# Optimization experiments

Hardware: AMD Instinct MI355X
Metric: run time of the kernel (lower is better)

## Reference

```python
import jax, jax.numpy as jnp
import numpy as np

N_USER = 20000
N_ITEM = 20000
N = N_USER + N_ITEM          # total nodes
D = 128                      # n_hid (= in_feats = out_feats)
H = 4                        # GAT heads
L = 2                        # n_layers
M = 8                        # mem_size (hypernet bottleneck)
T = 5                        # num_rels in MemoryLayer
E_UI = 40000                 # user->item bipartite edges
E_T = 16000                  # homogeneous edges per relation type (grouped)
EPS = 1e-5


def _layer_norm(x, w, b):
    mu = x.mean(-1, keepdims=True)
    var = ((x - mu) ** 2).mean(-1, keepdims=True)
    return (x - mu) * jax.lax.rsqrt(var + EPS) * w + b


def _gat(h_src, h_dst, src_idx, dst_idx, n_dst, W, al, ar, bias):
    """DGL GATConv (shared fc, eval-mode dropout=identity, elu activation)."""
    fs = (h_src @ W.T).reshape(-1, H, D)          # [Ns, H, D]
    fd = (h_dst @ W.T).reshape(-1, H, D)          # [Nd, H, D]
    el = (fs * al).sum(-1)                        # [Ns, H]
    er = (fd * ar).sum(-1)                        # [Nd, H]
    e = jax.nn.leaky_relu(el[src_idx] + er[dst_idx], 0.2)   # [E, H]
    emax = jax.ops.segment_max(e, dst_idx, num_segments=n_dst)
    ex = jnp.exp(e - emax[dst_idx])
    denom = jax.ops.segment_sum(ex, dst_idx, num_segments=n_dst)
    a = ex / denom[dst_idx]                       # edge softmax per dst
    rst = jax.ops.segment_sum(a[:, :, None] * fs[src_idx], dst_idx, num_segments=n_dst)
    return jax.nn.elu(rst + bias.reshape(1, H, D))           # [Nd, H, D]


def _memory_layer(feat, edge_src, edge_dst, Wc, bc, Ww, nWc, nbc, nWw, h_bias, ln_w, ln_b):
    # edges grouped by relation type: edge_src/edge_dst are [T, E_T]
    hs = feat[edge_src]                           # [T, Et, D]
    hd = feat[edge_dst]                           # [T, Et, D]
    # per-edge hypernetwork: coef = LeakyReLU(Linear(dst)); w = Ww(coef); msg = w @ src
    coef = jax.nn.leaky_relu(jnp.einsum('ted,tmd->tem', hd, Wc) + bc[:, None, :], 0.2)
    tmp = jnp.einsum('tei,tmoi->temo', hs, Ww)    # [T, Et, M, D] -- M-bottleneck path
    msg = jnp.einsum('tem,temo->teo', coef, tmp)  # [T, Et, D]
    flat_dst = edge_dst.reshape(-1)
    s = jax.ops.segment_sum(msg.reshape(-1, D), flat_dst, num_segments=N)
    cnt = jax.ops.segment_sum(jnp.ones((flat_dst.shape[0],), feat.dtype), flat_dst, num_segments=N)
    agg = s / jnp.maximum(cnt, 1.0)[:, None]      # fn.mean (0 for isolated nodes)
    rep = _layer_norm(agg, ln_w, ln_b) + h_bias
    # self-loop node_ME(feat, feat)
    ncoef = jax.nn.leaky_relu(feat @ nWc.T + nbc, 0.2)       # [N, M]
    ntmp = jnp.einsum('ni,moi->nmo', feat, nWw)              # [N, M, D]
    rep = rep + jnp.einsum('nm,nmo->no', ncoef, ntmp)
    return jax.nn.leaky_relu(rep, 0.2)            # dropout = identity (eval)


def setup_inputs() -> dict:
    key = jax.random.key(0)
    ks = jax.random.split(key, 16)
    s = 0.05
    return {
        "embedding": jax.random.normal(ks[0], (N, D), jnp.float32),
        "gat_fc_W": jax.random.normal(ks[1], (L, 2, H * D, D), jnp.float32) * s,
        "gat_attn_l": jax.random.normal(ks[2], (L, 2, H, D), jnp.float32) * s,
        "gat_attn_r": jax.random.normal(ks[3], (L, 2, H, D), jnp.float32) * s,
        "gat_bias": jnp.zeros((L, 2, H * D), jnp.float32),
        "proj_W": jax.random.normal(ks[4], (L, 2, D, H * D), jnp.float32) * s,
        "proj_b": jnp.zeros((L, 2, D), jnp.float32),
        "mem_rel_Wc": jax.random.normal(ks[5], (L, T, M, D), jnp.float32) * s,
        "mem_rel_bc": jnp.zeros((L, T, M), jnp.float32),
        "mem_rel_Ww": jax.random.normal(ks[6], (L, T, M, D, D), jnp.float32) * s,
        "mem_node_Wc": jax.random.normal(ks[7], (L, M, D), jnp.float32) * s,
        "mem_node_bc": jnp.zeros((L, M), jnp.float32),
        "mem_node_Ww": jax.random.normal(ks[8], (L, M, D, D), jnp.float32) * s,
        "mem_h_bias": jnp.zeros((L, D), jnp.float32),
        "mem_ln_w": jnp.ones((L, D), jnp.float32),
        "mem_ln_b": jnp.zeros((L, D), jnp.float32),
        "final_ln_w": jnp.ones(((L + 1) * D,), jnp.float32),
        "final_ln_b": jnp.zeros(((L + 1) * D,), jnp.float32),
        "src_u": jax.random.randint(ks[9], (E_UI,), 0, N_USER, jnp.int32),
        "dst_i": jax.random.randint(ks[10], (E_UI,), 0, N_ITEM, jnp.int32),
        "edge_src": jax.random.randint(ks[11], (T, E_T), 0, N, jnp.int32),
        "edge_dst": jax.random.randint(ks[12], (T, E_T), 0, N, jnp.int32),
    }


def reference(embedding, gat_fc_W, gat_attn_l, gat_attn_r, gat_bias, proj_W, proj_b,
              mem_rel_Wc, mem_rel_bc, mem_rel_Ww, mem_node_Wc, mem_node_bc, mem_node_Ww,
              mem_h_bias, mem_ln_w, mem_ln_b, final_ln_w, final_ln_b,
              src_u, dst_i, edge_src, edge_dst):
    features = embedding
    all_emb = [features]
    for l in range(L):
        hu, hi = features[:N_USER], features[N_USER:]
        # relation 0: item -> user (dst = user)
        gu = _gat(hi, hu, dst_i, src_u, N_USER,
                  gat_fc_W[l, 0], gat_attn_l[l, 0], gat_attn_r[l, 0], gat_bias[l, 0])
        ru = jax.nn.elu(gu.reshape(N_USER, H * D) @ proj_W[l, 0].T + proj_b[l, 0])
        # relation 1: user -> item (dst = item)
        gi = _gat(hu, hi, src_u, dst_i, N_ITEM,
                  gat_fc_W[l, 1], gat_attn_l[l, 1], gat_attn_r[l, 1], gat_bias[l, 1])
        ri = jnp.asarray(jax.nn.elu(gi.reshape(N_ITEM, H * D) @ proj_W[l, 1].T + proj_b[l, 1]))
        trans = jnp.concatenate([ru, ri], axis=0)             # [N, D]
        mem = _memory_layer(all_emb[-1], edge_src, edge_dst,
                            mem_rel_Wc[l], mem_rel_bc[l], mem_rel_Ww[l],
                            mem_node_Wc[l], mem_node_bc[l], mem_node_Ww[l],
                            mem_h_bias[l], mem_ln_w[l], mem_ln_b[l])
        features = mem + trans
        all_emb.append(features)
    return _layer_norm(jnp.concatenate(all_emb, axis=1), final_ln_w, final_ln_b)
```

## Files before the change

kernel.cpp:

```cpp
#include <hip/hip_runtime.h>
#include <hip/hip_bf16.h>
#include <math.h>

typedef __hip_bfloat16 bf16;

#define NUSER 20000
#define NITEM 20000
#define NTOT  40000
#define DD    128
#define HH    4
#define TT    5
#define MMEM  8
#define EUI   40000
#define ET    16000

#define MP_N  40064
#define MP_H  20096

typedef __attribute__((ext_vector_type(8))) short short8;
typedef __attribute__((ext_vector_type(4))) float f32x4;

__device__ __forceinline__ void gload16(const bf16* g, bf16* l){
  __builtin_amdgcn_global_load_lds(
      (const __attribute__((address_space(1))) unsigned int*)g,
      (__attribute__((address_space(3))) unsigned int*)l, 16, 0, 0);
}
__device__ __forceinline__ float bu2f_lo(unsigned u){ return __uint_as_float(u << 16); }
__device__ __forceinline__ float bu2f_hi(unsigned u){ return __uint_as_float(u & 0xffff0000u); }

__device__ __forceinline__ int stage_cg(int lane){
  return (((lane&3) ^ ((lane>>2)&3) ^ (lane>>4)) << 3);
}
__device__ __forceinline__ int read_pc8(int lm, int lq){
  return ((lq ^ (lm&3) ^ ((lm>>2)&3)) << 3);
}

__global__ __launch_bounds__(256) void k_mfma_gemm(
    const bf16* __restrict__ A, const bf16* __restrict__ B,
    const float* __restrict__ bias, float* __restrict__ C,
    long Astr, long Bstr, long biasStr, long Cstr,
    int ldc, int M, int K, int act, int accum)
{
  A += (size_t)blockIdx.z*Astr; B += (size_t)blockIdx.z*Bstr;
  if (bias) bias += (size_t)blockIdx.z*biasStr;
  C += (size_t)blockIdx.z*Cstr;
  __shared__ bf16 As[3][4096];
  __shared__ bf16 Bs[3][4096];
  int tid = threadIdx.x;
  int wave = tid >> 6, lane = tid & 63;
  int r0 = blockIdx.x * 128, c0 = blockIdx.y * 128;
  int wm = (wave >> 1) * 64, wn = (wave & 1) * 64;
  f32x4 acc[4][4];
  #pragma unroll
  for (int i=0;i<4;i++)
    #pragma unroll
    for (int j=0;j<4;j++) acc[i][j] = (f32x4){0.f,0.f,0.f,0.f};

  int rq = lane >> 2;
  int cg = stage_cg(lane);
  const bf16* Ag = A + (size_t)(r0 + wave*32 + rq)*K + cg;
  const bf16* Bg = B + (size_t)(c0 + wave*32 + rq)*K + cg;
  int lm = lane & 15, lq = lane >> 4;
  int pc8 = read_pc8(lm, lq);

  int ns = K >> 5;
  {
    bf16* dA = &As[0][wave*1024]; bf16* dB = &Bs[0][wave*1024];
    gload16(Ag,        dA); gload16(Ag + 16*K, dA + 512);
    gload16(Bg,        dB); gload16(Bg + 16*K, dB + 512);
  }
  if (ns > 1){
    bf16* dA = &As[1][wave*1024]; bf16* dB = &Bs[1][wave*1024];
    gload16(Ag + 32,        dA); gload16(Ag + 16*K + 32, dA + 512);
    gload16(Bg + 32,        dB); gload16(Bg + 16*K + 32, dB + 512);
    asm volatile("s_waitcnt vmcnt(4)" ::: "memory");
  } else {
    asm volatile("s_waitcnt vmcnt(0)" ::: "memory");
  }
  __builtin_amdgcn_s_barrier();

  int cur = 0, stg = 2;
  for (int i = 0; i < ns; i++){
    if (i + 2 < ns){
      int k2 = (i + 2) << 5;
      bf16* dA = &As[stg][wave*1024]; bf16* dB = &Bs[stg][wave*1024];
      gload16(Ag + k2,        dA); gload16(Ag + 16*K + k2, dA + 512);
      gload16(Bg + k2,        dB); gload16(Bg + 16*K + k2, dB + 512);
    }
    const bf16* Ard = &As[cur][(wm + lm)*32 + pc8];
    const bf16* Brd = &Bs[cur][(wn + lm)*32 + pc8];
    short8 af[4], bfv[4];
    #pragma unroll
    for (int ii=0;ii<4;ii++) af[ii]  = *(const short8*)(Ard + ii*16*32);
    #pragma unroll
    for (int j=0;j<4;j++)    bfv[j]  = *(const short8*)(Brd + j*16*32);
    #pragma unroll
    for (int ii=0;ii<4;ii++)
      #pragma unroll
      for (int j=0;j<4;j++)
        acc[ii][j] = __builtin_amdgcn_mfma_f32_16x16x32_bf16(af[ii], bfv[j], acc[ii][j], 0, 0, 0);
    if (i < ns - 1){
      if (i + 2 < ns) asm volatile("s_waitcnt vmcnt(4)" ::: "memory");
      else            asm volatile("s_waitcnt vmcnt(0)" ::: "memory");
      __builtin_amdgcn_s_barrier();
    }
    cur = (cur == 2) ? 0 : cur + 1;
    stg = (stg == 2) ? 0 : stg + 1;
  }
  #pragma unroll
  for (int i=0;i<4;i++){
    #pragma unroll
    for (int j=0;j<4;j++){
      int c = c0 + wn + j*16 + lm;
      #pragma unroll
      for (int rg=0; rg<4; rg++){
        int r = r0 + wm + i*16 + lq*4 + rg;
        if (r < M){
          float v = acc[i][j][rg];
          if (bias) v += bias[c];
          if (act==1) v = v>0.f ? v : expm1f(v);
          float* cp = &C[(size_t)r*ldc + c];
          if (accum) *cp += v; else *cp = v;
        }
      }
    }
  }
}

__global__ __launch_bounds__(256) void k_fc_gemm(
    const bf16* __restrict__ A, const bf16* __restrict__ B,
    bf16* __restrict__ Fb, const float* __restrict__ al, const float* __restrict__ ar,
    float* __restrict__ el, float* __restrict__ er, int M)
{
  __shared__ bf16 As[3][4096];
  __shared__ bf16 Bs[3][4096];
  __shared__ float redE[2][2][128];
  int tid = threadIdx.x;
  int wave = tid >> 6, lane = tid & 63;
  int h = blockIdx.y;
  int r0 = blockIdx.x * 128;
  int wm = (wave >> 1) * 64, wn = (wave & 1) * 64;
  f32x4 acc[4][4];
  #pragma unroll
  for (int i=0;i<4;i++)
    #pragma unroll
    for (int j=0;j<4;j++) acc[i][j] = (f32x4){0.f,0.f,0.f,0.f};

  int rq = lane >> 2;
  int cg = stage_cg(lane);
  const bf16* Ag = A + (size_t)(r0 + wave*32 + rq)*128 + cg;
  const bf16* Bg = B + (size_t)(h*128 + wave*32 + rq)*128 + cg;
  int lm = lane & 15, lq = lane >> 4;
  int pc8 = read_pc8(lm, lq);

  {
    bf16* dA = &As[0][wave*1024]; bf16* dB = &Bs[0][wave*1024];
    gload16(Ag,            dA); gload16(Ag + 16*128, dA + 512);
    gload16(Bg,            dB); gload16(Bg + 16*128, dB + 512);
  }
  {
    bf16* dA = &As[1][wave*1024]; bf16* dB = &Bs[1][wave*1024];
    gload16(Ag + 32,       dA); gload16(Ag + 16*128 + 32, dA + 512);
    gload16(Bg + 32,       dB); gload16(Bg + 16*128 + 32, dB + 512);
  }
  asm volatile("s_waitcnt vmcnt(4)" ::: "memory");
  __builtin_amdgcn_s_barrier();

  #pragma unroll
  for (int i = 0; i < 4; i++){
    if (i + 2 < 4){
      const int k2 = (i + 2) << 5;
      bf16* dA = &As[(i+2)%3][wave*1024]; bf16* dB = &Bs[(i+2)%3][wave*1024];
      gload16(Ag + k2,        dA); gload16(Ag + 16*128 + k2, dA + 512);
      gload16(Bg + k2,        dB); gload16(Bg + 16*128 + k2, dB + 512);
    }
    const bf16* Ard = &As[i%3][(wm + lm)*32 + pc8];
    const bf16* Brd = &Bs[i%3][(wn + lm)*32 + pc8];
    short8 af[4], bfv[4];
    #pragma unroll
    for (int ii=0;ii<4;ii++) af[ii]  = *(const short8*)(Ard + ii*16*32);
    #pragma unroll
    for (int j=0;j<4;j++)    bfv[j]  = *(const short8*)(Brd + j*16*32);
    #pragma unroll
    for (int ii=0;ii<4;ii++)
      #pragma unroll
      for (int j=0;j<4;j++)
        acc[ii][j] = __builtin_amdgcn_mfma_f32_16x16x32_bf16(af[ii], bfv[j], acc[ii][j], 0, 0, 0);
    if (i < 3){
      if (i + 2 < 4) asm volatile("s_waitcnt vmcnt(4)" ::: "memory");
      else           asm volatile("s_waitcnt vmcnt(0)" ::: "memory");
      __builtin_amdgcn_s_barrier();
    }
  }
  float alv[4], arv[4];
  #pragma unroll
  for (int j=0;j<4;j++){
    int c = h*128 + wn + j*16 + lm;
    alv[j] = al[c]; arv[j] = ar[c];
  }
  int wnh = wave & 1;
  #pragma unroll
  for (int i=0;i<4;i++){
    #pragma unroll
    for (int rg=0; rg<4; rg++){
      float se = 0.f, sr = 0.f;
      #pragma unroll
      for (int j=0;j<4;j++){
        float v = acc[i][j][rg];
        se = fmaf(v, alv[j], se);
        sr = fmaf(v, arv[j], sr);
      }
      #pragma unroll
      for (int msk=1; msk<16; msk<<=1){
        se += __shfl_xor(se, msk);
        sr += __shfl_xor(sr, msk);
      }
      if (lm == 0){
        int rl = wm + i*16 + lq*4 + rg;
        redE[0][wnh][rl] = se;
        redE[1][wnh][rl] = sr;
      }
    }
  }
  #pragma unroll
  for (int i=0;i<4;i++){
    #pragma unroll
    for (int j=0;j<4;j++){
      int c = h*128 + wn + j*16 + lm;
      #pragma unroll
      for (int rg=0; rg<4; rg++){
        int r = r0 + wm + i*16 + lq*4 + rg;
        if (r < M) Fb[(size_t)r*512 + c] = __float2bfloat16(acc[i][j][rg]);
      }
    }
  }
  __syncthreads();
  if (tid < 128){
    int r = r0 + tid;
    if (r < M) el[(size_t)r*4 + h] = redE[0][0][tid] + redE[0][1][tid];
  } else {
    int t2 = tid - 128;
    int r = r0 + t2;
    if (r < M) er[(size_t)r*4 + h] = redE[1][0][t2] + redE[1][1][t2];
  }
}

__global__ __launch_bounds__(256) void k_memgemm(
    const float* __restrict__ feat, const int* __restrict__ src,
    const float* __restrict__ coef, const bf16* __restrict__ B,
    float* __restrict__ C, bf16* __restrict__ Cb,
    const float* __restrict__ trans, float* __restrict__ fout,
    long srcStr, long coefStr, long Bstr, long CbStr,
    int Mvalid, int mode)
{
  __shared__ bf16 Af[64*136];
  __shared__ float cfS[8*64];
  __shared__ bf16 Bs[3][2][4096];
  int t = blockIdx.y;
  const int*   srcT  = src ? src + (size_t)t*srcStr : nullptr;
  const float* coefT = coef + (size_t)t*coefStr;
  const bf16*  Bt    = B + (size_t)t*Bstr;
  int tid = threadIdx.x, wave = tid >> 6, lane = tid & 63;
  int r0 = blockIdx.x * 64;

  {
    int rL = tid >> 2, seg = tid & 3;
    int r = r0 + rL;
    bool valid = r < Mvalid;
    int s = valid ? (srcT ? srcT[r] : r) : 0;
    const float4* fp = (const float4*)(feat + (size_t)s*128 + seg*32);
    bf16* ap = Af + rL*136 + seg*32;
    #pragma unroll
    for (int q=0;q<8;q+=2){
      float4 v0 = fp[q], v1 = fp[q+1];
      *(__hip_bfloat162*)(ap + q*4)     = __float22bfloat162_rn(make_float2(v0.x, v0.y));
      *(__hip_bfloat162*)(ap + q*4 + 2) = __float22bfloat162_rn(make_float2(v0.z, v0.w));
      *(__hip_bfloat162*)(ap + q*4 + 4) = __float22bfloat162_rn(make_float2(v1.x, v1.y));
      *(__hip_bfloat162*)(ap + q*4 + 6) = __float22bfloat162_rn(make_float2(v1.z, v1.w));
    }
  }
  if (tid < 64){
    int r = r0 + tid;
    bool valid = r < Mvalid;
    #pragma unroll
    for (int m=0;m<8;m++)
      cfS[m*64 + tid] = valid ? coefT[(size_t)r*8 + m] : 0.f;
  }

  int rq = lane >> 2;
  int cg = stage_cg(lane);
  const bf16* Bg0 = Bt + (size_t)(wave*32 + rq)*1024 + cg;
  const bf16* Bg1 = Bt + (size_t)(wave*32 + 16 + rq)*1024 + cg;
  int wm = (wave >> 1) * 32, wn = (wave & 1) * 64;
  int lm = lane & 15, lq = lane >> 4;
  int pc8 = read_pc8(lm, lq);

  #pragma unroll
  for (int p0=0; p0<2; p0++){
    #pragma unroll
    for (int h=0; h<2; h++){
      int kk = p0*2 + h;
      bf16* d = &Bs[p0][h][wave*1024];
      gload16(Bg0 + kk*32, d);
      gload16(Bg1 + kk*32, d + 512);
    }
  }
  asm volatile("s_waitcnt lgkmcnt(0) vmcnt(4)" ::: "memory");
  __builtin_amdgcn_s_barrier();

  short8 afr[4][2];
  #pragma unroll
  for (int ic=0; ic<4; ic++)
    #pragma unroll
    for (int i=0; i<2; i++)
      afr[ic][i] = *(const short8*)(Af + (size_t)(wm + i*16 + lm)*136 + ic*32 + lq*8);

  f32x4 accC[2][4];
  #pragma unroll
  for (int i=0;i<2;i++)
    #pragma unroll
    for (int j=0;j<4;j++) accC[i][j] = (f32x4){0.f,0.f,0.f,0.f};
  f32x4 accM[2][4];

  #pragma unroll
  for (int p = 0; p < 16; p++){
    if (p + 2 < 16){
      #pragma unroll
      for (int h=0; h<2; h++){
        const int kk = (p+2)*2 + h;
        bf16* d = &Bs[(p+2)%3][h][wave*1024];
        gload16(Bg0 + kk*32, d);
        gload16(Bg1 + kk*32, d + 512);
      }
    }
    #pragma unroll
    for (int h=0; h<2; h++){
      const int kk = p*2 + h;
      const int ic = kk & 3;
      const bf16* bb = &Bs[p%3][h][0];
      short8 bfv[4];
      #pragma unroll
      for (int j=0;j<4;j++)
        bfv[j] = *(const short8*)(bb + (wn + lm + j*16)*32 + pc8);
      if (ic == 0){
        #pragma unroll
        for (int i=0;i<2;i++)
          #pragma unroll
          for (int j=0;j<4;j++)
            accM[i][j] = __builtin_amdgcn_mfma_f32_16x16x32_bf16(afr[0][i], bfv[j],
                             (f32x4){0.f,0.f,0.f,0.f}, 0, 0, 0);
      } else {
        #pragma unroll
        for (int i=0;i<2;i++)
          #pragma unroll
          for (int j=0;j<4;j++)
            accM[i][j] = __builtin_amdgcn_mfma_f32_16x16x32_bf16(afr[ic][i], bfv[j], accM[i][j], 0, 0, 0);
      }
    }
    if (p & 1){
      const int m = p >> 1;
      #pragma unroll
      for (int i=0;i<2;i++){
        f32x4 cf4 = *(const f32x4*)(cfS + m*64 + wm + i*16 + lq*4);
        #pragma unroll
        for (int j=0;j<4;j++)
          #pragma unroll
          for (int rg=0; rg<4; rg++)
            accC[i][j][rg] = fmaf(cf4[rg], accM[i][j][rg], accC[i][j][rg]);
      }
    }
    if (p < 15){
      if (p + 2 < 16) asm volatile("s_waitcnt vmcnt(4)" ::: "memory");
      else            asm volatile("s_waitcnt vmcnt(0)" ::: "memory");
      __builtin_amdgcn_s_barrier();
    }
  }

  #pragma unroll
  for (int i=0;i<2;i++){
    #pragma unroll
    for (int j=0;j<4;j++){
      int c = wn + j*16 + lm;
      #pragma unroll
      for (int rg=0; rg<4; rg++){
        int r = r0 + wm + i*16 + lq*4 + rg;
        if (r < Mvalid){
          float v = accC[i][j][rg];
          if (mode == 0){
            Cb[(size_t)t*CbStr + (size_t)r*128 + c] = __float2bfloat16(v);
          } else {
            float x = C[(size_t)r*128 + c] + v;
            x = x>0.f ? x : 0.2f*x;
            fout[(size_t)r*128 + c] = x + trans[(size_t)r*128 + c];
          }
        }
      }
    }
  }
}

__global__ void k_f2b(const float* __restrict__ in, bf16* __restrict__ o, int nv, int nt){
  int i = blockIdx.x*256 + threadIdx.x;
  if (i < nt) o[i] = __float2bfloat16(i < nv ? in[i] : 0.f);
}

__global__ void k_repack(const float* __restrict__ in, bf16* __restrict__ o){
  int s = blockIdx.y;
  int g = blockIdx.x*256 + threadIdx.x;
  int m = g >> 14, od = (g >> 7) & 127, i = g & 127;
  o[(size_t)s*131072 + (size_t)od*1024 + m*128 + i] = __float2bfloat16(in[(size_t)s*131072 + g]);
}

__global__ void k_hist(const int* __restrict__ dIdx, int* __restrict__ cnt, int E){
  int e = blockIdx.x*256+threadIdx.x;
  if (e<E) atomicAdd(&cnt[dIdx[e]], 1);
}

__global__ __launch_bounds__(1024) void k_scan(const int* __restrict__ in,
                                               int* __restrict__ out, int n){
  __shared__ int wsum[16];
  __shared__ int carry;
  int tidx = threadIdx.x, lane = tidx & 63, w = tidx >> 6;
  if (tidx == 0) carry = 0;
  __syncthreads();
  for (int base = 0; base < n; base += 1024){
    int i = base + tidx;
    int v = (i < n) ? in[i] : 0;
    int x = v;
    #pragma unroll
    for (int off = 1; off < 64; off <<= 1){
      int t = __shfl_up(x, off);
      if (lane >= off) x += t;
    }
    if (lane == 63) wsum[w] = x;
    __syncthreads();
    if (w == 0 && lane < 16){
      int t = wsum[lane];
      #pragma unroll
      for (int off=1; off<16; off<<=1){
        int u = __shfl_up(t, off, 16);
        if (lane >= off) t += u;
      }
      wsum[lane] = t;
    }
    __syncthreads();
    int woff = (w == 0) ? 0 : wsum[w-1];
    int excl = carry + woff + x - v;
    if (i < n) out[i] = excl;
    __syncthreads();
    if (tidx == 1023) carry = carry + wsum[15];
    __syncthreads();
  }
  if (tidx == 0) out[n] = carry;
}

__global__ void k_csr_scatter(const int* __restrict__ sIdx, const int* __restrict__ dIdx,
                              int sOff, const int* __restrict__ rowptr,
                              int* __restrict__ cursor, int* __restrict__ col, int E){
  int e = blockIdx.x*256+threadIdx.x; if (e>=E) return;
  int d = dIdx[e];
  int pos = rowptr[d] + atomicAdd(&cursor[d], 1);
  col[pos] = sIdx[e] + sOff;
}

__global__ void k_csr_scatter_eid(const int* __restrict__ dIdx, const int* __restrict__ rowptr,
                                  int* __restrict__ cursor, int* __restrict__ col, int E){
  int e = blockIdx.x*256+threadIdx.x; if (e>=E) return;
  int d = dIdx[e];
  int pos = rowptr[d] + atomicAdd(&cursor[d], 1);
  col[pos] = e;
}

__global__ __launch_bounds__(64) void k_gat_gather(
    const int* __restrict__ rowptr, const int* __restrict__ col,
    const float* __restrict__ el, const float* __restrict__ er,
    const bf16* __restrict__ Fb, const float* __restrict__ gb,
    bf16* __restrict__ rstb, int dOff)
{
  int dl = blockIdx.x;
  int lane = threadIdx.x;
  int h = lane >> 4;
  int off = (lane & 15) << 3;
  float erh = er[(size_t)(dl + dOff)*4 + h];
  float m = -INFINITY, den = 0.f;
  float acc[8];
  #pragma unroll
  for (int i=0;i<8;i++) acc[i]=0.f;
  int jb = rowptr[dl], je = rowptr[dl+1];
  for (int j=jb; j<je; j++){
    int s = col[j];
    float e = el[(size_t)s*4+h] + erh;
    e = e > 0.f ? e : 0.2f*e;
    float mn = fmaxf(m, e);
    float sc = __expf(m - mn);
    float wj = __expf(e - mn);
    den = den*sc + wj;
    m = mn;
    uint4 u = *(const uint4*)(Fb + (size_t)s*512 + h*128 + off);
    acc[0]=acc[0]*sc + wj*bu2f_lo(u.x); acc[1]=acc[1]*sc + wj*bu2f_hi(u.x);
    acc[2]=acc[2]*sc + wj*bu2f_lo(u.y); acc[3]=acc[3]*sc + wj*bu2f_hi(u.y);
    acc[4]=acc[4]*sc + wj*bu2f_lo(u.z); acc[5]=acc[5]*sc + wj*bu2f_hi(u.z);
    acc[6]=acc[6]*sc + wj*bu2f_lo(u.w); acc[7]=acc[7]*sc + wj*bu2f_hi(u.w);
  }
  float inv = den > 0.f ? 1.f/den : 0.f;
  int cb = h*128 + off;
  float x[8];
  #pragma unroll
  for (int q=0;q<8;q++){
    float v = acc[q]*inv + gb[cb+q];
    x[q] = v>0.f ? v : expm1f(v);
  }
  union { uint4 u; __hip_bfloat162 p[4]; } O;
  #pragma unroll
  for (int q=0;q<4;q++) O.p[q] = __float22bfloat162_rn(make_float2(x[2*q], x[2*q+1]));
  *(uint4*)(rstb + (size_t)dl*512 + cb) = O.u;
}

__global__ void k_coef(const float* __restrict__ feat, const int* __restrict__ idx,
                       const float* __restrict__ Wc, const float* __restrict__ bc,
                       float* __restrict__ outc, int cnt){
  int t = blockIdx.y;
  __shared__ float wT[DD*MMEM];
  __shared__ float bS[MMEM];
  for (int i=threadIdx.x;i<MMEM*DD;i+=128){
    int m = i >> 7, d = i & 127;
    wT[d*MMEM + m] = Wc[(size_t)t*MMEM*DD + i];
  }
  if (threadIdx.x < MMEM) bS[threadIdx.x] = bc[t*MMEM + threadIdx.x];
  __syncthreads();
  int e = blockIdx.x*128 + threadIdx.x; if (e >= cnt) return;
  int node = idx ? idx[(size_t)t*cnt + e] : e;
  float acc[MMEM];
  #pragma unroll
  for (int m=0;m<MMEM;m++) acc[m]=bS[m];
  const float4* fr = (const float4*)(feat + (size_t)node*DD);
  for (int d4=0; d4<32; d4++){
    float4 v = fr[d4];
    const float* w0 = wT + d4*4*MMEM;
    #pragma unroll
    for (int m=0;m<MMEM;m++) acc[m] = fmaf(v.x, w0[m], acc[m]);
    #pragma unroll
    for (int m=0;m<MMEM;m++) acc[m] = fmaf(v.y, w0[MMEM+m], acc[m]);
    #pragma unroll
    for (int m=0;m<MMEM;m++) acc[m] = fmaf(v.z, w0[2*MMEM+m], acc[m]);
    #pragma unroll
    for (int m=0;m<MMEM;m++) acc[m] = fmaf(v.w, w0[3*MMEM+m], acc[m]);
  }
  float* op = outc + ((size_t)t*cnt + e)*MMEM;
  #pragma unroll
  for (int m=0;m<MMEM;m++){ float v=acc[m]; op[m] = v>0.f ? v : 0.2f*v; }
}

__global__ void k_mem_gather(const int* __restrict__ rpT, const int* __restrict__ colT,
                             const bf16* __restrict__ msg, float* __restrict__ sAgg){
  int n = blockIdx.x*4 + (threadIdx.x >> 6);
  if (n >= NTOT) return;
  int lane = threadIdx.x & 63;
  int jb = rpT[n], je = rpT[n+1];
  float a0=0.f, a1=0.f;
  for (int j=jb;j<je;j++){
    unsigned u = ((const unsigned*)(msg + (size_t)colT[j]*128))[lane];
    a0 += bu2f_lo(u); a1 += bu2f_hi(u);
  }
  *(float2*)(sAgg + (size_t)n*128 + lane*2) = make_float2(a0, a1);
}

__global__ void k_memln(const float* __restrict__ s, const int* __restrict__ rpT,
                        const float* __restrict__ lw, const float* __restrict__ lb,
                        const float* __restrict__ hb, float* __restrict__ outp){
  int n = blockIdx.x, lane = threadIdx.x;
  float c = fmaxf((float)(rpT[n+1]-rpT[n]), 1.f);
  float x1 = s[(size_t)n*128+lane]/c, x2 = s[(size_t)n*128+64+lane]/c;
  float t = x1+x2;
  #pragma unroll
  for (int off=32;off;off>>=1) t += __shfl_xor(t,off);
  float mu = t * (1.f/128.f);
  float d1=x1-mu, d2=x2-mu;
  float v = d1*d1+d2*d2;
  #pragma unroll
  for (int off=32;off;off>>=1) v += __shfl_xor(v,off);
  float r = rsqrtf(v*(1.f/128.f) + 1e-5f);
  outp[(size_t)n*128+lane]    = d1*r*lw[lane]    + lb[lane]    + hb[lane];
  outp[(size_t)n*128+64+lane] = d2*r*lw[64+lane] + lb[64+lane] + hb[64+lane];
}

__global__ void k_final_ln(const float* __restrict__ emb, const float* __restrict__ f1,
                           const float* __restrict__ f2, const float* __restrict__ w,
                           const float* __restrict__ b, float* __restrict__ out){
  int n = blockIdx.x, t = threadIdx.x;
  __shared__ float red[4];
  float x0 = emb[(size_t)n*128+t];
  float x1 = f1[(size_t)n*128+t];
  float x2 = f2[(size_t)n*128+t];
  float s = x0+x1+x2;
  #pragma unroll
  for (int off=32;off;off>>=1) s += __shfl_xor(s,off);
  if ((t&63)==0) red[t>>6] = s;
  __syncthreads();
  float mu = (red[0]+red[1]) * (1.f/384.f);
  float d0=x0-mu, d1=x1-mu, d2=x2-mu;
  float v = d0*d0+d1*d1+d2*d2;
  #pragma unroll
  for (int off=32;off;off>>=1) v += __shfl_xor(v,off);
  if ((t&63)==0) red[2+(t>>6)] = v;
  __syncthreads();
  float var = (red[2]+red[3]) * (1.f/384.f);
  float r = rsqrtf(var + 1e-5f);
  size_t o = (size_t)n*384;
  out[o+t]     = d0*r*w[t]     + b[t];
  out[o+128+t] = d1*r*w[128+t] + b[128+t];
  out[o+256+t] = d2*r*w[256+t] + b[256+t];
}

extern "C" void kernel_launch(void* const* d_in, const int* in_sizes, int n_in,
                              void* d_out, int out_size, void* d_ws, size_t ws_size,
                              hipStream_t stream)
{
  const float* emb   = (const float*)d_in[0];
  const float* fcW   = (const float*)d_in[1];
  const float* attl  = (const float*)d_in[2];
  const float* attr  = (const float*)d_in[3];
  const float* gbias = (const float*)d_in[4];
  const float* projW = (const float*)d_in[5];
  const float* projB = (const float*)d_in[6];
  const float* relWc = (const float*)d_in[7];
  const float* relbc = (const float*)d_in[8];
  const float* relWw = (const float*)d_in[9];
  const float* nodWc = (const float*)d_in[10];
  const float* nodbc = (const float*)d_in[11];
  const float* nodWw = (const float*)d_in[12];
  const float* hbias = (const float*)d_in[13];
  const float* mlnw  = (const float*)d_in[14];
  const float* mlnb  = (const float*)d_in[15];
  const float* flnw  = (const float*)d_in[16];
  const float* flnb  = (const float*)d_in[17];
  const int*  srcU  = (const int*)d_in[18];
  const int*  dstI  = (const int*)d_in[19];
  const int*  eSrc  = (const int*)d_in[20];
  const int*  eDst  = (const int*)d_in[21];
  float* out = (float*)d_out;

  char* wp = (char*)d_ws;
  auto alloc = [&](size_t bytes)->void* {
    void* p = (void*)wp; wp += (bytes + 511) & ~(size_t)511; return p;
  };
  float* feat1 = (float*)alloc((size_t)NTOT*DD*4);
  float* feat2 = (float*)alloc((size_t)NTOT*DD*4);
  float* Fbuf  = (float*)alloc((size_t)NTOT*512*4);
  float* rst   = (float*)alloc((size_t)NTOT*DD*2*4);
  bf16*  rstb0 = (bf16*)alloc((size_t)2*MP_H*512*2);
  float* trans = (float*)alloc((size_t)NTOT*DD*4);
  float* elF   = (float*)alloc((size_t)NTOT*4*4);
  float* erF   = (float*)alloc((size_t)NTOT*4*4);
  int* rpA  = (int*)alloc((size_t)(NUSER+1)*4);
  int* colA = (int*)alloc((size_t)EUI*4);
  int* rpB  = (int*)alloc((size_t)(NITEM+1)*4);
  int* colB = (int*)alloc((size_t)EUI*4);
  int* icnt = (int*)alloc((size_t)20000*4);
  int* icur = (int*)alloc((size_t)20000*4);
  int* rpT  = (int*)alloc((size_t)(NTOT+1)*4);
  int* colT = (int*)alloc((size_t)TT*ET*4);
  int* cntT = (int*)alloc((size_t)NTOT*4);
  int* icurT= (int*)alloc((size_t)NTOT*4);
  bf16* featb  = (bf16*)alloc((size_t)MP_N*DD*2);
  bf16* fcWb   = (bf16*)alloc((size_t)4*512*DD*2);
  bf16* projWb = (bf16*)alloc((size_t)4*DD*512*2);
  bf16* relWwb = (bf16*)alloc((size_t)10*DD*1024*2);
  bf16* nodWwb = (bf16*)alloc((size_t)2*DD*1024*2);
  bf16*  Fb     = (bf16*)Fbuf;
  bf16*  msgBb  = (bf16*)((char*)Fbuf + (size_t)NTOT*512*2);
  float* coefB  = (float*)((char*)msgBb + (size_t)TT*ET*128*2);
  float* ncoefB = coefB + (size_t)TT*ET*8;
  bf16*  rstb1  = rstb0 + (size_t)MP_H*512;
  float* sAgg   = rst;
  float* memO   = rst + (size_t)NTOT*DD;

  k_f2b<<<dim3((4*512*DD+255)/256),256,0,stream>>>(fcW, fcWb, 4*512*DD, 4*512*DD);
  k_f2b<<<dim3((4*DD*512+255)/256),256,0,stream>>>(projW, projWb, 4*DD*512, 4*DD*512);
  k_repack<<<dim3(512,10),256,0,stream>>>(relWw, relWwb);
  k_repack<<<dim3(512,2),256,0,stream>>>(nodWw, nodWwb);
  hipMemsetAsync(rstb0 + (size_t)20000*512, 0, (size_t)(MP_H-20000)*512*2, stream);
  hipMemsetAsync(rstb1 + (size_t)20000*512, 0, (size_t)(MP_H-20000)*512*2, stream);

  hipMemsetAsync(icnt, 0, 20000*4, stream);
  hipMemsetAsync(icur, 0, 20000*4, stream);
  k_hist<<<dim3((EUI+255)/256),256,0,stream>>>(srcU, icnt, EUI);
  k_scan<<<dim3(1),1024,0,stream>>>(icnt, rpA, NUSER);
  k_csr_scatter<<<dim3((EUI+255)/256),256,0,stream>>>(dstI, srcU, NUSER, rpA, icur, colA, EUI);
  hipMemsetAsync(icnt, 0, 20000*4, stream);
  hipMemsetAsync(icur, 0, 20000*4, stream);
  k_hist<<<dim3((EUI+255)/256),256,0,stream>>>(dstI, icnt, EUI);
  k_scan<<<dim3(1),1024,0,stream>>>(icnt, rpB, NITEM);
  k_csr_scatter<<<dim3((EUI+255)/256),256,0,stream>>>(srcU, dstI, 0, rpB, icur, colB, EUI);
  hipMemsetAsync(cntT, 0, NTOT*4, stream);
  hipMemsetAsync(icurT, 0, NTOT*4, stream);
  k_hist<<<dim3((TT*ET+255)/256),256,0,stream>>>(eDst, cntT, TT*ET);
  k_scan<<<dim3(1),1024,0,stream>>>(cntT, rpT, NTOT);
  k_csr_scatter_eid<<<dim3((TT*ET+255)/256),256,0,stream>>>(eDst, rpT, icurT, colT, TT*ET);

  const float* feats[3] = {emb, feat1, feat2};
  for (int l=0; l<2; l++){
    const float* fin  = feats[l];
    float* fout = (float*)feats[l+1];

    k_f2b<<<dim3((MP_N*DD+255)/256),256,0,stream>>>(fin, featb, NTOT*DD, MP_N*DD);

    for (int d=0; d<2; d++){
      k_fc_gemm<<<dim3(MP_N/128, 4),256,0,stream>>>(
          featb, fcWb + (size_t)(l*2+d)*512*DD, Fb,
          attl+(size_t)(l*2+d)*512, attr+(size_t)(l*2+d)*512, elF, erF, NTOT);
      int dOff = (d==0) ? 0 : NUSER;
      const int* rp  = (d==0) ? rpA : rpB;
      const int* col = (d==0) ? colA : colB;
      k_gat_gather<<<dim3(20000),64,0,stream>>>(rp, col, elF, erF, Fb,
          gbias+(size_t)(l*2+d)*512, (d==0) ? rstb0 : rstb1, dOff);
    }
    k_mfma_gemm<<<dim3(MP_H/128, 1, 2),256,0,stream>>>(
        rstb0, projWb + (size_t)(l*2)*DD*512, projB + (size_t)(l*2)*DD, trans,
        (long)MP_H*512, (long)DD*512, (long)DD, (long)20000*DD,
        DD, 20000, 512, 1, 0);

    k_coef<<<dim3((ET+127)/128, TT),128,0,stream>>>(fin, eDst,
        relWc+(size_t)l*TT*MMEM*DD, relbc+(size_t)l*TT*MMEM, coefB, ET);
    k_memgemm<<<dim3(ET/64, TT),256,0,stream>>>(
        fin, eSrc, coefB, relWwb + (size_t)l*TT*DD*1024,
        nullptr, msgBb, nullptr, nullptr,
        (long)ET, (long)ET*8, (long)DD*1024, (long)ET*128, ET, 0);
    k_mem_gather<<<dim3(NTOT/4),256,0,stream>>>(rpT, colT, msgBb, sAgg);
    k_memln<<<dim3(NTOT),64,0,stream>>>(sAgg, rpT, mlnw+(size_t)l*DD, mlnb+(size_t)l*DD,
                                        hbias+(size_t)l*DD, memO);
    k_coef<<<dim3((NTOT+127)/128, 1),128,0,stream>>>(fin, nullptr,
        nodWc+(size_t)l*MMEM*DD, nodbc+(size_t)l*MMEM, ncoefB, NTOT);
    k_memgemm<<<dim3(MP_N/64, 1),256,0,stream>>>(
        fin, nullptr, ncoefB, nodWwb + (size_t)l*DD*1024,
        memO, nullptr, trans, fout,
        0, 0, 0, 0, NTOT, 2);
  }

  k_final_ln<<<dim3(NTOT),128,0,stream>>>(emb, feat1, feat2, flnw, flnb, out);
}
```

Baseline: 899.6 us.

## Give each wave a private B staging ring in k_memgemm, removing block barriers

```diff
diff --git a/kernel.cpp b/kernel.cpp
--- a/kernel.cpp
+++ b/kernel.cpp
@@ -255,7 +255,7 @@
 {
   __shared__ bf16 Af[64*136];
   __shared__ float cfS[8*64];
-  __shared__ bf16 Bs[3][2][4096];
+  __shared__ bf16 Bs[3][4][2048];
   int t = blockIdx.y;
   const int*   srcT  = src ? src + (size_t)t*srcStr : nullptr;
   const float* coefT = coef + (size_t)t*coefStr;
@@ -289,23 +289,27 @@
 
   int rq = lane >> 2;
   int cg = stage_cg(lane);
-  const bf16* Bg0 = Bt + (size_t)(wave*32 + rq)*1024 + cg;
-  const bf16* Bg1 = Bt + (size_t)(wave*32 + 16 + rq)*1024 + cg;
   int wm = (wave >> 1) * 32, wn = (wave & 1) * 64;
   int lm = lane & 15, lq = lane >> 4;
   int pc8 = read_pc8(lm, lq);
 
-  #pragma unroll
-  for (int p0=0; p0<2; p0++){
-    #pragma unroll
-    for (int h=0; h<2; h++){
-      int kk = p0*2 + h;
-      bf16* d = &Bs[p0][h][wave*1024];
-      gload16(Bg0 + kk*32, d);
-      gload16(Bg1 + kk*32, d + 512);
-    }
-  }
-  asm volatile("s_waitcnt lgkmcnt(0) vmcnt(4)" ::: "memory");
+  const bf16* Bg0 = Bt + (size_t)(wn +  0 + rq)*1024 + cg;
+  const bf16* Bg1 = Bt + (size_t)(wn + 16 + rq)*1024 + cg;
+  const bf16* Bg2 = Bt + (size_t)(wn + 32 + rq)*1024 + cg;
+  const bf16* Bg3 = Bt + (size_t)(wn + 48 + rq)*1024 + cg;
+
+#define ISSUE_B(kk) do{                          \
+    bf16* _d = &Bs[(kk)%3][wave][0];             \
+    gload16(Bg0 + (kk)*32, _d);                  \
+    gload16(Bg1 + (kk)*32, _d + 512);            \
+    gload16(Bg2 + (kk)*32, _d + 1024);           \
+    gload16(Bg3 + (kk)*32, _d + 1536);           \
+  }while(0)
+
+  ISSUE_B(0);
+  ISSUE_B(1);
+
+  asm volatile("s_waitcnt lgkmcnt(0)" ::: "memory");
   __builtin_amdgcn_s_barrier();
 
   short8 afr[4][2];
@@ -323,42 +327,33 @@
   f32x4 accM[2][4];
 
   #pragma unroll
-  for (int p = 0; p < 16; p++){
-    if (p + 2 < 16){
-      #pragma unroll
-      for (int h=0; h<2; h++){
-        const int kk = (p+2)*2 + h;
-        bf16* d = &Bs[(p+2)%3][h][wave*1024];
-        gload16(Bg0 + kk*32, d);
-        gload16(Bg1 + kk*32, d + 512);
-      }
-    }
-    #pragma unroll
-    for (int h=0; h<2; h++){
-      const int kk = p*2 + h;
-      const int ic = kk & 3;
-      const bf16* bb = &Bs[p%3][h][0];
-      short8 bfv[4];
-      #pragma unroll
-      for (int j=0;j<4;j++)
-        bfv[j] = *(const short8*)(bb + (wn + lm + j*16)*32 + pc8);
-      if (ic == 0){
+  for (int kk = 0; kk < 32; kk++){
+    if (kk + 2 < 32) ISSUE_B(kk+2);
+    if (kk + 2 < 32)      asm volatile("s_waitcnt vmcnt(8)" ::: "memory");
+    else if (kk + 1 < 32) asm volatile("s_waitcnt vmcnt(4)" ::: "memory");
+    else                  asm volatile("s_waitcnt vmcnt(0)" ::: "memory");
+    const int ic = kk & 3;
+    const bf16* bb = &Bs[kk%3][wave][0];
+    short8 bfv[4];
+    #pragma unroll
+    for (int j=0;j<4;j++)
+      bfv[j] = *(const short8*)(bb + j*512 + lm*32 + pc8);
+    if (ic == 0){
+      #pragma unroll
+      for (int i=0;i<2;i++)
         #pragma unroll
-        for (int i=0;i<2;i++)
-          #pragma unroll
-          for (int j=0;j<4;j++)
-            accM[i][j] = __builtin_amdgcn_mfma_f32_16x16x32_bf16(afr[0][i], bfv[j],
-                             (f32x4){0.f,0.f,0.f,0.f}, 0, 0, 0);
-      } else {
+        for (int j=0;j<4;j++)
+          accM[i][j] = __builtin_amdgcn_mfma_f32_16x16x32_bf16(afr[0][i], bfv[j],
+                           (f32x4){0.f,0.f,0.f,0.f}, 0, 0, 0);
+    } else {
+      #pragma unroll
+      for (int i=0;i<2;i++)
         #pragma unroll
-        for (int i=0;i<2;i++)
-          #pragma unroll
-          for (int j=0;j<4;j++)
-            accM[i][j] = __builtin_amdgcn_mfma_f32_16x16x32_bf16(afr[ic][i], bfv[j], accM[i][j], 0, 0, 0);
-      }
-    }
-    if (p & 1){
-      const int m = p >> 1;
+        for (int j=0;j<4;j++)
+          accM[i][j] = __builtin_amdgcn_mfma_f32_16x16x32_bf16(afr[ic][i], bfv[j], accM[i][j], 0, 0, 0);
+    }
+    if (ic == 3){
+      const int m = kk >> 2;
       #pragma unroll
       for (int i=0;i<2;i++){
         f32x4 cf4 = *(const f32x4*)(cfS + m*64 + wm + i*16 + lq*4);
@@ -369,12 +364,8 @@
             accC[i][j][rg] = fmaf(cf4[rg], accM[i][j][rg], accC[i][j][rg]);
       }
     }
-    if (p < 15){
-      if (p + 2 < 16) asm volatile("s_waitcnt vmcnt(4)" ::: "memory");
-      else            asm volatile("s_waitcnt vmcnt(0)" ::: "memory");
-      __builtin_amdgcn_s_barrier();
-    }
-  }
+  }
+#undef ISSUE_B
 
   #pragma unroll
   for (int i=0;i<2;i++){
```

New measurement: 887.9 us. No clear change (-1.3%).
